# Performance work log

Measured on AMD Instinct MI355X. Metric: run time of the kernel, lower is better.

The kernel has to match this reference:

```python
import jax, jax.numpy as jnp
import numpy as np

N_NODES = 100000
N_EDGES = 1600000
D_IN = 32
D_OUT = 64


def setup_inputs() -> dict:
    key = jax.random.key(0)
    ks = jax.random.split(key, 6)
    x = jax.random.normal(ks[0], (N_NODES, D_IN), dtype=jnp.float32)
    edge_row = jax.random.randint(ks[1], (N_EDGES,), 0, N_NODES, dtype=jnp.int32)
    edge_col = jax.random.randint(ks[2], (N_EDGES,), 0, N_NODES, dtype=jnp.int32)
    edge_val = jax.random.uniform(ks[3], (N_EDGES,), dtype=jnp.float32)
    W = jax.random.normal(ks[4], (D_IN, D_OUT), dtype=jnp.float32) * (1.0 / np.sqrt(D_IN))
    b = jax.random.normal(ks[5], (D_OUT,), dtype=jnp.float32) * 0.01
    return {"x": x, "edge_row": edge_row, "edge_col": edge_col,
            "edge_val": edge_val, "W": W, "b": b, "k": 4}


def _spmm(edge_row, edge_col, edge_val, x, n_nodes):
    # out[i] = sum_{e: row[e]==i} val[e] * x[col[e]]  (sparse adj @ x)
    gathered = edge_val[:, None] * x[edge_col]  # [E, D]
    return jax.ops.segment_sum(gathered, edge_row, num_segments=n_nodes)


def reference(x, edge_row, edge_col, edge_val, W, b, k):
    # k-hop propagation: x <- A @ x, repeated k times (k is a static Python int)
    for _ in range(k):
        x = _spmm(edge_row, edge_col, edge_val, x, N_NODES)
    # final dense linear: x @ W + b
    return x @ W + b
```

## Files before the change

kernel.cpp:

```cpp
#include <hip/hip_runtime.h>
#include <hip/hip_fp16.h>

#define N_NODES 100000
#define N_EDGES 1600000
#define D_IN 32
#define D_OUT 64

#define RPB 200
#define NBKT 500
#define CAP 4096
#define EPT 16
#define SCT 256
#define EPB (EPT * SCT)
#define SBLOCKS ((N_EDGES + EPB - 1) / EPB)
#define N2 (N_NODES * D_IN / 2)
#define CVT_BLOCKS ((N2 + 255) / 256)

#define COL_BITS 17
#define COL_MASK ((1u << COL_BITS) - 1u)
#define VAL_SCALE 32767.0f
#define VAL_INV (1.0f / 32767.0f)

typedef unsigned int uv2 __attribute__((ext_vector_type(2)));
typedef unsigned int uv4 __attribute__((ext_vector_type(4)));

__global__ void init_bcur(int* __restrict__ bcur) {
    int i = threadIdx.x;
    if (i < NBKT) bcur[i] = i * CAP;
}

__global__ void scatter_chunks(const int* __restrict__ erow,
                               const int* __restrict__ ecol,
                               const float* __restrict__ eval_,
                               int* __restrict__ bcur,
                               int2* __restrict__ staged,
                               const float2* __restrict__ xf,
                               unsigned int* __restrict__ xh) {
    if (blockIdx.x >= SBLOCKS) {
        int i = (blockIdx.x - SBLOCKS) * blockDim.x + threadIdx.x;
        if (i < N2) {
            float2 f = xf[i];
            __half2 h = __floats2half2_rn(f.x, f.y);
            xh[i] = *(unsigned int*)&h;
        }
        return;
    }
    __shared__ int h[NBKT];
    __shared__ int cb[NBKT];
    for (int i = threadIdx.x; i < NBKT; i += blockDim.x) h[i] = 0;
    __syncthreads();
    int base = blockIdx.x * EPB;
    unsigned pk[EPT]; float val[EPT]; int brk[EPT];
#pragma unroll
    for (int k = 0; k < EPT; ++k) {
        int e = base + k * SCT + threadIdx.x;
        if (e < N_EDGES) {
            int r = __builtin_nontemporal_load(&erow[e]);
            int c = __builtin_nontemporal_load(&ecol[e]);
            float v = __builtin_nontemporal_load(&eval_[e]);
            int b = r / RPB;
            int rl = r - b * RPB;
            int rank = atomicAdd(&h[b], 1);
            pk[k] = ((unsigned)rl << COL_BITS) | (unsigned)c;
            val[k] = v;
            brk[k] = b | (rank << 9);
        } else brk[k] = -1;
    }
    __syncthreads();
    for (int i = threadIdx.x; i < NBKT; i += blockDim.x) {
        int c = h[i];
        if (c) cb[i] = atomicAdd(&bcur[i], c);
    }
    __syncthreads();
#pragma unroll
    for (int k = 0; k < EPT; ++k) {
        if (brk[k] >= 0) {
            int b = brk[k] & 511;
            int rank = brk[k] >> 9;
            int2 p; p.x = (int)pk[k]; p.y = __float_as_int(val[k]);
            staged[cb[b] + rank] = p;
        }
    }
}

__global__ void sort_bucket(const int* __restrict__ bcur,
                            const int2* __restrict__ staged,
                            unsigned int* __restrict__ epack,
                            int2* __restrict__ row_rng) {
    __shared__ int hist[RPB];
    __shared__ int offs[RPB];
    __shared__ int cur[RPB];
    __shared__ int ptot;
    int b = blockIdx.x;
    int s0 = b * CAP, s1 = bcur[b];
    for (int i = threadIdx.x; i < RPB; i += blockDim.x) hist[i] = 0;
    __syncthreads();
    for (int e = s0 + threadIdx.x; e < s1; e += blockDim.x) {
        unsigned w = (unsigned)staged[e].x;
        atomicAdd(&hist[w >> COL_BITS], 1);
    }
    __syncthreads();
    if (threadIdx.x == 0) {
        int run = 0;
        for (int i = 0; i < RPB; ++i) {
            offs[i] = run;
            run += (hist[i] + 7) & ~7;
        }
        ptot = run;
    }
    __syncthreads();
    int r0 = b * RPB;
    int pt = ptot;
    for (int i = threadIdx.x; i < pt; i += blockDim.x) epack[s0 + i] = 0u;
    for (int i = threadIdx.x; i < RPB; i += blockDim.x) {
        int st = s0 + offs[i];
        int2 rr; rr.x = st; rr.y = st + ((hist[i] + 7) & ~7);
        row_rng[r0 + i] = rr;
        cur[i] = offs[i];
    }
    __syncthreads();
    for (int e = s0 + threadIdx.x; e < s1; e += blockDim.x) {
        int2 p = staged[e];
        unsigned w = (unsigned)p.x;
        int rl = (int)(w >> COL_BITS);
        int pos = atomicAdd(&cur[rl], 1);
        float v = __int_as_float(p.y);
        unsigned q = (unsigned)(int)(v * VAL_SCALE + 0.5f);
        epack[s0 + pos] = (q << COL_BITS) | (w & COL_MASK);
    }
}

__global__ void spmm_csr(const int2* __restrict__ row_rng,
                         const uv4* __restrict__ epack4,
                         const uv2* __restrict__ xin,
                         uv2* __restrict__ xout) {
    int lane = threadIdx.x & 63;
    int wave = threadIdx.x >> 6;
    int qt = lane >> 4;
    int g  = (lane >> 3) & 1;
    int j  = lane & 7;
    int r = (blockIdx.x * (blockDim.x >> 6) + wave) * 4 + qt;
    if (r >= N_NODES) return;
    int2 pe = row_rng[r];
    int p0 = pe.x, p1 = pe.y;
    float4 a0 = {0.f,0.f,0.f,0.f}, a1 = {0.f,0.f,0.f,0.f};
    float4 a2 = {0.f,0.f,0.f,0.f}, a3 = {0.f,0.f,0.f,0.f};
    for (int eb = p0; eb < p1; eb += 8) {
        uv4 q = epack4[(eb >> 2) + g];
        unsigned q0 = q.x, q1 = q.y, q2 = q.z, q3 = q.w;
        uv2 w0 = xin[(q0 & COL_MASK) * 8 + j];
        uv2 w1 = xin[(q1 & COL_MASK) * 8 + j];
        uv2 w2 = xin[(q2 & COL_MASK) * 8 + j];
        uv2 w3 = xin[(q3 & COL_MASK) * 8 + j];
        float v0 = (float)(q0 >> COL_BITS) * VAL_INV;
        float v1 = (float)(q1 >> COL_BITS) * VAL_INV;
        float v2 = (float)(q2 >> COL_BITS) * VAL_INV;
        float v3 = (float)(q3 >> COL_BITS) * VAL_INV;
        unsigned w0x = w0.x, w0y = w0.y, w1x = w1.x, w1y = w1.y;
        unsigned w2x = w2.x, w2y = w2.y, w3x = w3.x, w3y = w3.y;
        float2 f0a = __half22float2(*(__half2*)&w0x), f0b = __half22float2(*(__half2*)&w0y);
        float2 f1a = __half22float2(*(__half2*)&w1x), f1b = __half22float2(*(__half2*)&w1y);
        float2 f2a = __half22float2(*(__half2*)&w2x), f2b = __half22float2(*(__half2*)&w2y);
        float2 f3a = __half22float2(*(__half2*)&w3x), f3b = __half22float2(*(__half2*)&w3y);
        a0.x += v0 * f0a.x; a0.y += v0 * f0a.y; a0.z += v0 * f0b.x; a0.w += v0 * f0b.y;
        a1.x += v1 * f1a.x; a1.y += v1 * f1a.y; a1.z += v1 * f1b.x; a1.w += v1 * f1b.y;
        a2.x += v2 * f2a.x; a2.y += v2 * f2a.y; a2.z += v2 * f2b.x; a2.w += v2 * f2b.y;
        a3.x += v3 * f3a.x; a3.y += v3 * f3a.y; a3.z += v3 * f3b.x; a3.w += v3 * f3b.y;
    }
    float4 acc;
    acc.x = (a0.x + a1.x) + (a2.x + a3.x);
    acc.y = (a0.y + a1.y) + (a2.y + a3.y);
    acc.z = (a0.z + a1.z) + (a2.z + a3.z);
    acc.w = (a0.w + a1.w) + (a2.w + a3.w);
    acc.x += __shfl_xor(acc.x, 8, 64);
    acc.y += __shfl_xor(acc.y, 8, 64);
    acc.z += __shfl_xor(acc.z, 8, 64);
    acc.w += __shfl_xor(acc.w, 8, 64);
    if (g == 0) {
        __half2 o0 = __floats2half2_rn(acc.x, acc.y);
        __half2 o1 = __floats2half2_rn(acc.z, acc.w);
        uv2 w;
        w.x = *(unsigned int*)&o0;
        w.y = *(unsigned int*)&o1;
        xout[r * 8 + j] = w;
    }
}

__global__ void linear_bias(const __half2* __restrict__ xin,
                            const float* __restrict__ W,
                            const float* __restrict__ b,
                            float* __restrict__ out) {
    __shared__ float sW[D_IN * D_OUT];
    __shared__ float sb[D_OUT];
    for (int i = threadIdx.x; i < D_IN * D_OUT; i += blockDim.x) sW[i] = W[i];
    if (threadIdx.x < D_OUT) sb[threadIdx.x] = b[threadIdx.x];
    __syncthreads();

    int r = blockIdx.x * 4 + (threadIdx.x >> 6);
    int j = threadIdx.x & 63;
    if (r >= N_NODES) return;

    const __half2* xr = xin + r * (D_IN / 2);
    float acc = sb[j];
#pragma unroll
    for (int d = 0; d < D_IN / 2; ++d) {
        float2 f = __half22float2(xr[d]);
        acc += f.x * sW[(2 * d) * D_OUT + j] + f.y * sW[(2 * d + 1) * D_OUT + j];
    }
    out[r * D_OUT + j] = acc;
}

extern "C" void kernel_launch(void* const* d_in, const int* in_sizes, int n_in,
                              void* d_out, int out_size, void* d_ws, size_t ws_size,
                              hipStream_t stream) {
    const float* x     = (const float*)d_in[0];
    const int*   erow  = (const int*)d_in[1];
    const int*   ecol  = (const int*)d_in[2];
    const float* eval_ = (const float*)d_in[3];
    const float* W     = (const float*)d_in[4];
    const float* b     = (const float*)d_in[5];
    float* out = (float*)d_out;

    unsigned int* xh0 = (unsigned int*)d_ws;
    unsigned int* xh1 = xh0 + (size_t)N2;
    int* bcur = (int*)(xh1 + (size_t)N2);
    int2* row_rng = (int2*)(bcur + 512);
    int2* staged = row_rng + N_NODES;
    unsigned int* epack = (unsigned int*)(staged + (size_t)NBKT * CAP);

    const int threads = 256;

    init_bcur<<<1, 512, 0, stream>>>(bcur);
    scatter_chunks<<<SBLOCKS + CVT_BLOCKS, SCT, 0, stream>>>(
        erow, ecol, eval_, bcur, staged, (const float2*)x, xh0);
    sort_bucket<<<NBKT, threads, 0, stream>>>(bcur, staged, epack, row_rng);

    const int rows_per_block = (threads / 64) * 4;
    const int sblocks = (N_NODES + rows_per_block - 1) / rows_per_block;
    const unsigned int* cur = xh0;
    for (int hop = 0; hop < 4; ++hop) {
        unsigned int* dst = (hop & 1) ? xh0 : xh1;
        spmm_csr<<<sblocks, threads, 0, stream>>>((const int2*)row_rng,
                                                  (const uv4*)epack,
                                                  (const uv2*)cur, (uv2*)dst);
        cur = dst;
    }

    const int lin_blocks = (N_NODES + 3) / 4;
    linear_bias<<<lin_blocks, 256, 0, stream>>>((const __half2*)cur, W, b, out);
}
```

Before: 243.4 us.

## Group rows by padded length class to balance SpMM wavefront work

Rows are binned into length classes (padded edge count / 8) in sort_bucket. A new perm_scatter kernel builds a permutation so that rows of similar length sit next to each other. spmm_csr then reads row ranges through this permutation and writes to the original row index, so the four rows sharing a wave have similar trip counts and less divergence. The cost is an extra kernel, a 16-byte per-row permutation read, and scattered output writes. CAP is also raised, which enlarges the staged and epack buffers.

```diff
diff --git a/kernel.cpp b/kernel.cpp
--- a/kernel.cpp
+++ b/kernel.cpp
@@ -8,13 +8,14 @@
 
 #define RPB 200
 #define NBKT 500
-#define CAP 4096
+#define CAP 4608
 #define EPT 16
 #define SCT 256
 #define EPB (EPT * SCT)
 #define SBLOCKS ((N_EDGES + EPB - 1) / EPB)
 #define N2 (N_NODES * D_IN / 2)
 #define CVT_BLOCKS ((N2 + 255) / 256)
+#define NCLS 64
 
 #define COL_BITS 17
 #define COL_MASK ((1u << COL_BITS) - 1u)
@@ -24,9 +25,11 @@
 typedef unsigned int uv2 __attribute__((ext_vector_type(2)));
 typedef unsigned int uv4 __attribute__((ext_vector_type(4)));
 
-__global__ void init_bcur(int* __restrict__ bcur) {
+__global__ void init_bcur(int* __restrict__ bcur,
+                          int* __restrict__ gclass, int* __restrict__ gcur) {
     int i = threadIdx.x;
     if (i < NBKT) bcur[i] = i * CAP;
+    if (i < NCLS) { gclass[i] = 0; gcur[i] = 0; }
 }
 
 __global__ void scatter_chunks(const int* __restrict__ erow,
@@ -86,14 +89,17 @@
 __global__ void sort_bucket(const int* __restrict__ bcur,
                             const int2* __restrict__ staged,
                             unsigned int* __restrict__ epack,
-                            int2* __restrict__ row_rng) {
+                            int2* __restrict__ row_rng,
+                            int* __restrict__ gclass) {
     __shared__ int hist[RPB];
     __shared__ int offs[RPB];
     __shared__ int cur[RPB];
+    __shared__ int ccnt[NCLS];
     __shared__ int ptot;
     int b = blockIdx.x;
     int s0 = b * CAP, s1 = bcur[b];
     for (int i = threadIdx.x; i < RPB; i += blockDim.x) hist[i] = 0;
+    if (threadIdx.x < NCLS) ccnt[threadIdx.x] = 0;
     __syncthreads();
     for (int e = s0 + threadIdx.x; e < s1; e += blockDim.x) {
         unsigned w = (unsigned)staged[e].x;
@@ -113,12 +119,19 @@
     int pt = ptot;
     for (int i = threadIdx.x; i < pt; i += blockDim.x) epack[s0 + i] = 0u;
     for (int i = threadIdx.x; i < RPB; i += blockDim.x) {
+        int pd = (hist[i] + 7) & ~7;
         int st = s0 + offs[i];
-        int2 rr; rr.x = st; rr.y = st + ((hist[i] + 7) & ~7);
+        int2 rr; rr.x = st; rr.y = st + pd;
         row_rng[r0 + i] = rr;
         cur[i] = offs[i];
-    }
-    __syncthreads();
+        int cls = min(NCLS - 1, pd >> 3);
+        atomicAdd(&ccnt[cls], 1);
+    }
+    __syncthreads();
+    if (threadIdx.x < NCLS) {
+        int c = ccnt[threadIdx.x];
+        if (c) atomicAdd(&gclass[threadIdx.x], c);
+    }
     for (int e = s0 + threadIdx.x; e < s1; e += blockDim.x) {
         int2 p = staged[e];
         unsigned w = (unsigned)p.x;
@@ -130,7 +143,42 @@
     }
 }
 
-__global__ void spmm_csr(const int2* __restrict__ row_rng,
+__global__ void perm_scatter(const int2* __restrict__ row_rng,
+                             const int* __restrict__ gclass,
+                             int* __restrict__ gcur,
+                             int4* __restrict__ prow) {
+    __shared__ int gc[NCLS];
+    __shared__ int base[NCLS];
+    __shared__ int h[NCLS];
+    __shared__ int cb[NCLS];
+    int t = threadIdx.x;
+    if (t < NCLS) { h[t] = 0; gc[t] = gclass[t]; }
+    __syncthreads();
+    int r = blockIdx.x * blockDim.x + t;
+    int cls = 0, rank = 0; int2 rr;
+    bool valid = (r < N_NODES);
+    if (valid) {
+        rr = row_rng[r];
+        cls = min(NCLS - 1, (rr.y - rr.x) >> 3);
+        rank = atomicAdd(&h[cls], 1);
+    }
+    __syncthreads();
+    if (t < NCLS) {
+        int s = 0;
+        for (int i = 0; i < t; ++i) s += gc[i];
+        base[t] = s;
+        int c = h[t];
+        cb[t] = c ? atomicAdd(&gcur[t], c) : 0;
+    }
+    __syncthreads();
+    if (valid) {
+        int pos = base[cls] + cb[cls] + rank;
+        int4 p; p.x = rr.x; p.y = rr.y; p.z = r; p.w = 0;
+        prow[pos] = p;
+    }
+}
+
+__global__ void spmm_csr(const int4* __restrict__ prow,
                          const uv4* __restrict__ epack4,
                          const uv2* __restrict__ xin,
                          uv2* __restrict__ xout) {
@@ -139,10 +187,10 @@
     int qt = lane >> 4;
     int g  = (lane >> 3) & 1;
     int j  = lane & 7;
-    int r = (blockIdx.x * (blockDim.x >> 6) + wave) * 4 + qt;
-    if (r >= N_NODES) return;
-    int2 pe = row_rng[r];
-    int p0 = pe.x, p1 = pe.y;
+    int idx = (blockIdx.x * (blockDim.x >> 6) + wave) * 4 + qt;
+    if (idx >= N_NODES) return;
+    int4 pr = prow[idx];
+    int p0 = pr.x, p1 = pr.y, outr = pr.z;
     float4 a0 = {0.f,0.f,0.f,0.f}, a1 = {0.f,0.f,0.f,0.f};
     float4 a2 = {0.f,0.f,0.f,0.f}, a3 = {0.f,0.f,0.f,0.f};
     for (int eb = p0; eb < p1; eb += 8) {
@@ -182,7 +230,7 @@
         uv2 w;
         w.x = *(unsigned int*)&o0;
         w.y = *(unsigned int*)&o1;
-        xout[r * 8 + j] = w;
+        xout[outr * 8 + j] = w;
     }
 }
 
@@ -224,23 +272,28 @@
     unsigned int* xh0 = (unsigned int*)d_ws;
     unsigned int* xh1 = xh0 + (size_t)N2;
     int* bcur = (int*)(xh1 + (size_t)N2);
-    int2* row_rng = (int2*)(bcur + 512);
-    int2* staged = row_rng + N_NODES;
+    int* gclass = bcur + 512;
+    int* gcur = gclass + NCLS;
+    int2* row_rng = (int2*)(gcur + NCLS);
+    int4* prow = (int4*)(row_rng + N_NODES);
+    int2* staged = (int2*)(prow + N_NODES);
     unsigned int* epack = (unsigned int*)(staged + (size_t)NBKT * CAP);
 
     const int threads = 256;
 
-    init_bcur<<<1, 512, 0, stream>>>(bcur);
+    init_bcur<<<1, 512, 0, stream>>>(bcur, gclass, gcur);
     scatter_chunks<<<SBLOCKS + CVT_BLOCKS, SCT, 0, stream>>>(
         erow, ecol, eval_, bcur, staged, (const float2*)x, xh0);
-    sort_bucket<<<NBKT, threads, 0, stream>>>(bcur, staged, epack, row_rng);
+    sort_bucket<<<NBKT, threads, 0, stream>>>(bcur, staged, epack, row_rng, gclass);
+    perm_scatter<<<(N_NODES + threads - 1) / threads, threads, 0, stream>>>(
+        row_rng, gclass, gcur, prow);
 
     const int rows_per_block = (threads / 64) * 4;
     const int sblocks = (N_NODES + rows_per_block - 1) / rows_per_block;
     const unsigned int* cur = xh0;
     for (int hop = 0; hop < 4; ++hop) {
         unsigned int* dst = (hop & 1) ? xh0 : xh1;
-        spmm_csr<<<sblocks, threads, 0, stream>>>((const int2*)row_rng,
+        spmm_csr<<<sblocks, threads, 0, stream>>>(prow,
                                                   (const uv4*)epack,
                                                   (const uv2*)cur, (uv2*)dst);
         cur = dst;
```

After: 256.3 us. +5.3%, slower.

## Split SpMM by column half into two passes for gather cache locality

Applied to the files above, without the earlier changes.

Edges inside each row are partitioned by whether the column index falls in the first or second half of the nodes, and each hop runs as two kernel passes, one per column half. Each pass gathers from only half of the feature table (about 3.2MB in fp16), which is meant to fit better in L2/MALL and cut gather misses. The second pass reads back the partial result and adds to it, and both passes use nontemporal stores. The cost is double the launches, an extra read-modify-write of the output, an extra fp16 rounding of the partial sum, more padding per row, and a larger bucket capacity.

```diff
diff --git a/kernel.cpp b/kernel.cpp
--- a/kernel.cpp
+++ b/kernel.cpp
@@ -5,10 +5,11 @@
 #define N_EDGES 1600000
 #define D_IN 32
 #define D_OUT 64
+#define NHALF 50000
 
 #define RPB 200
 #define NBKT 500
-#define CAP 4096
+#define CAP 5760
 #define EPT 16
 #define SCT 256
 #define EPB (EPT * SCT)
@@ -86,25 +87,31 @@
 __global__ void sort_bucket(const int* __restrict__ bcur,
                             const int2* __restrict__ staged,
                             unsigned int* __restrict__ epack,
-                            int2* __restrict__ row_rng) {
-    __shared__ int hist[RPB];
-    __shared__ int offs[RPB];
-    __shared__ int cur[RPB];
+                            int4* __restrict__ row_rng) {
+    __shared__ int hist0[RPB];
+    __shared__ int hist1[RPB];
+    __shared__ int offs0[RPB];
+    __shared__ int offs1[RPB];
+    __shared__ int cur0[RPB];
+    __shared__ int cur1[RPB];
     __shared__ int ptot;
     int b = blockIdx.x;
     int s0 = b * CAP, s1 = bcur[b];
-    for (int i = threadIdx.x; i < RPB; i += blockDim.x) hist[i] = 0;
+    for (int i = threadIdx.x; i < RPB; i += blockDim.x) { hist0[i] = 0; hist1[i] = 0; }
     __syncthreads();
     for (int e = s0 + threadIdx.x; e < s1; e += blockDim.x) {
         unsigned w = (unsigned)staged[e].x;
-        atomicAdd(&hist[w >> COL_BITS], 1);
+        if ((w & COL_MASK) < NHALF) atomicAdd(&hist0[w >> COL_BITS], 1);
+        else                        atomicAdd(&hist1[w >> COL_BITS], 1);
     }
     __syncthreads();
     if (threadIdx.x == 0) {
         int run = 0;
         for (int i = 0; i < RPB; ++i) {
-            offs[i] = run;
-            run += (hist[i] + 7) & ~7;
+            offs0[i] = run;
+            run += (hist0[i] + 7) & ~7;
+            offs1[i] = run;
+            run += (hist1[i] + 7) & ~7;
         }
         ptot = run;
     }
@@ -113,36 +120,41 @@
     int pt = ptot;
     for (int i = threadIdx.x; i < pt; i += blockDim.x) epack[s0 + i] = 0u;
     for (int i = threadIdx.x; i < RPB; i += blockDim.x) {
-        int st = s0 + offs[i];
-        int2 rr; rr.x = st; rr.y = st + ((hist[i] + 7) & ~7);
+        int rs = s0 + offs0[i];
+        int rm = s0 + offs1[i];
+        int re = rm + ((hist1[i] + 7) & ~7);
+        int4 rr; rr.x = rs; rr.y = rm; rr.z = re; rr.w = 0;
         row_rng[r0 + i] = rr;
-        cur[i] = offs[i];
+        cur0[i] = offs0[i];
+        cur1[i] = offs1[i];
     }
     __syncthreads();
     for (int e = s0 + threadIdx.x; e < s1; e += blockDim.x) {
         int2 p = staged[e];
         unsigned w = (unsigned)p.x;
         int rl = (int)(w >> COL_BITS);
-        int pos = atomicAdd(&cur[rl], 1);
+        int pos = ((w & COL_MASK) < NHALF) ? atomicAdd(&cur0[rl], 1)
+                                           : atomicAdd(&cur1[rl], 1);
         float v = __int_as_float(p.y);
         unsigned q = (unsigned)(int)(v * VAL_SCALE + 0.5f);
         epack[s0 + pos] = (q << COL_BITS) | (w & COL_MASK);
     }
 }
 
-__global__ void spmm_csr(const int2* __restrict__ row_rng,
-                         const uv4* __restrict__ epack4,
-                         const uv2* __restrict__ xin,
-                         uv2* __restrict__ xout) {
+__global__ void spmm_half(const int4* __restrict__ row_rng,
+                          const uv4* __restrict__ epack4,
+                          const uv2* __restrict__ xin,
+                          uv2* __restrict__ xout,
+                          int pass) {
     int lane = threadIdx.x & 63;
     int wave = threadIdx.x >> 6;
     int qt = lane >> 4;
     int g  = (lane >> 3) & 1;
     int j  = lane & 7;
     int r = (blockIdx.x * (blockDim.x >> 6) + wave) * 4 + qt;
-    if (r >= N_NODES) return;
-    int2 pe = row_rng[r];
-    int p0 = pe.x, p1 = pe.y;
+    int4 rr = row_rng[r];
+    int p0 = pass ? rr.y : rr.x;
+    int p1 = pass ? rr.z : rr.y;
     float4 a0 = {0.f,0.f,0.f,0.f}, a1 = {0.f,0.f,0.f,0.f};
     float4 a2 = {0.f,0.f,0.f,0.f}, a3 = {0.f,0.f,0.f,0.f};
     for (int eb = p0; eb < p1; eb += 8) {
@@ -177,12 +189,19 @@
     acc.z += __shfl_xor(acc.z, 8, 64);
     acc.w += __shfl_xor(acc.w, 8, 64);
     if (g == 0) {
+        if (pass) {
+            uv2 wp = __builtin_nontemporal_load(&xout[r * 8 + j]);
+            unsigned wpx = wp.x, wpy = wp.y;
+            float2 pa = __half22float2(*(__half2*)&wpx);
+            float2 pb = __half22float2(*(__half2*)&wpy);
+            acc.x += pa.x; acc.y += pa.y; acc.z += pb.x; acc.w += pb.y;
+        }
         __half2 o0 = __floats2half2_rn(acc.x, acc.y);
         __half2 o1 = __floats2half2_rn(acc.z, acc.w);
         uv2 w;
         w.x = *(unsigned int*)&o0;
         w.y = *(unsigned int*)&o1;
-        xout[r * 8 + j] = w;
+        __builtin_nontemporal_store(w, &xout[r * 8 + j]);
     }
 }
 
@@ -224,8 +243,8 @@
     unsigned int* xh0 = (unsigned int*)d_ws;
     unsigned int* xh1 = xh0 + (size_t)N2;
     int* bcur = (int*)(xh1 + (size_t)N2);
-    int2* row_rng = (int2*)(bcur + 512);
-    int2* staged = row_rng + N_NODES;
+    int4* row_rng = (int4*)(bcur + 512);
+    int2* staged = (int2*)(row_rng + N_NODES);
     unsigned int* epack = (unsigned int*)(staged + (size_t)NBKT * CAP);
 
     const int threads = 256;
@@ -236,13 +255,14 @@
     sort_bucket<<<NBKT, threads, 0, stream>>>(bcur, staged, epack, row_rng);
 
     const int rows_per_block = (threads / 64) * 4;
-    const int sblocks = (N_NODES + rows_per_block - 1) / rows_per_block;
+    const int sblocks = N_NODES / rows_per_block;
     const unsigned int* cur = xh0;
     for (int hop = 0; hop < 4; ++hop) {
         unsigned int* dst = (hop & 1) ? xh0 : xh1;
-        spmm_csr<<<sblocks, threads, 0, stream>>>((const int2*)row_rng,
-                                                  (const uv4*)epack,
-                                                  (const uv2*)cur, (uv2*)dst);
+        spmm_half<<<sblocks, threads, 0, stream>>>(row_rng, (const uv4*)epack,
+                                                   (const uv2*)cur, (uv2*)dst, 0);
+        spmm_half<<<sblocks, threads, 0, stream>>>(row_rng, (const uv4*)epack,
+                                                   (const uv2*)cur, (uv2*)dst, 1);
         cur = dst;
     }
 
```

Result: slower. 293.5 us (+20.6%).
